# Performance work log

Hardware: AMD Instinct MI355X
Metric: run time of the kernel (lower is better)

## Reference

```python
import jax, jax.numpy as jnp
import numpy as np

EMB_DIM = 2048
NHEADS = 16
KVHEADS = 4
D_KQ = 128
D_V = 128


def setup_inputs() -> dict:
    key = jax.random.key(0)
    ks = jax.random.split(key, 7)
    B, S = 2, 2048
    std = 0.02
    return {
        "q": jax.random.normal(ks[0], (B, S, EMB_DIM), jnp.float32),
        "k": jax.random.normal(ks[1], (B, S, EMB_DIM), jnp.float32),
        "v": jax.random.normal(ks[2], (B, S, EMB_DIM), jnp.float32),
        # weights stored [in, out] (transposed vs torch nn.Linear storage)
        "Wq": jax.random.normal(ks[3], (EMB_DIM, NHEADS * D_KQ), jnp.float32) * std,
        "Wk": jax.random.normal(ks[4], (EMB_DIM, KVHEADS * D_KQ), jnp.float32) * std,
        "Wv": jax.random.normal(ks[5], (EMB_DIM, KVHEADS * D_V), jnp.float32) * std,
        "Wo": jax.random.normal(ks[6], (NHEADS * D_V, EMB_DIM), jnp.float32) * std,
    }


def reference(q, k, v, Wq, Wk, Wv, Wo):
    B, S, _ = q.shape
    scale = D_KQ ** -0.25  # applied to both q and k -> combined 1/sqrt(d_kq)
    # per-head projections: [B, H, S, d]
    qh = (q @ Wq).reshape(B, S, NHEADS, D_KQ).transpose(0, 2, 1, 3) * scale
    kh = (k @ Wk).reshape(B, S, KVHEADS, D_KQ).transpose(0, 2, 1, 3) * scale
    vh = (v @ Wv).reshape(B, S, KVHEADS, D_V).transpose(0, 2, 1, 3)
    # GQA expansion: each kv head repeated `expansion` times consecutively
    expansion = NHEADS // KVHEADS
    kh = jnp.repeat(kh, expansion, axis=1)  # [B, H, S, d_kq]
    vh = jnp.repeat(vh, expansion, axis=1)  # [B, H, S, d_v]
    # full softmax FIRST, then causal tril mask, then renormalize (source quirk)
    scores = jax.nn.softmax(jnp.einsum("bhqd,bhkd->bhqk", qh, kh), axis=-1)
    scores = jnp.tril(scores)  # zero out strictly-upper triangle on last 2 dims
    scores = scores / (jnp.sum(scores, axis=-1, keepdims=True) + 1e-9)
    qkv = jnp.einsum("bhqk,bhkd->bhqd", scores, vh)  # [B, H, S, d_v]
    z = qkv.transpose(0, 2, 1, 3).reshape(B, S, NHEADS * D_V)
    return z @ Wo
```

## Files before the change

### kernel.cpp

```cpp
#include <hip/hip_runtime.h>

#define S_LEN 2048
#define EMB 2048
#define NH 16
#define KVH 4
#define DH 128

typedef __bf16 bf16x8 __attribute__((ext_vector_type(8)));
typedef float floatx4 __attribute__((ext_vector_type(4)));
typedef unsigned short ushortx8 __attribute__((ext_vector_type(8)));
typedef unsigned short ushortx4 __attribute__((ext_vector_type(4)));

static __device__ __forceinline__ unsigned short f2bf(float f) {
  unsigned u = __float_as_uint(f);
  return (unsigned short)((u + 0x7fffu + ((u >> 16) & 1u)) >> 16);
}

static __device__ __forceinline__ void gload16(const unsigned short* g, unsigned short* l) {
  __builtin_amdgcn_global_load_lds(
      (const __attribute__((address_space(1))) unsigned int*)(const void*)g,
      (__attribute__((address_space(3))) unsigned int*)(void*)l, 16, 0, 0);
}

__global__ __launch_bounds__(256) void pre_kernel(
    const float* __restrict__ q, const float* __restrict__ k, const float* __restrict__ v,
    const float* __restrict__ Wq, const float* __restrict__ Wk,
    const float* __restrict__ Wv, const float* __restrict__ Wo,
    unsigned short* __restrict__ qo, unsigned short* __restrict__ ko,
    unsigned short* __restrict__ vo,
    unsigned short* __restrict__ Wqt, unsigned short* __restrict__ Wkt,
    unsigned short* __restrict__ Wvt, unsigned short* __restrict__ Wot,
    float scale) {
  __shared__ float t[32][33];
  int bx = blockIdx.x;
  if (bx < 12288) {
    const int sel = bx >> 12;
    const float* in = (sel == 0) ? q : (sel == 1) ? k : v;
    unsigned short* out = (sel == 0) ? qo : (sel == 1) ? ko : vo;
    size_t i = (((size_t)(bx & 4095)) * 256 + threadIdx.x) * 8;
    floatx4 a = *(const floatx4*)(in + i);
    floatx4 bvec = *(const floatx4*)(in + i + 4);
    ushortx8 o;
    #pragma unroll
    for (int c = 0; c < 4; ++c) { o[c] = f2bf(a[c]); o[4 + c] = f2bf(bvec[c]); }
    *(ushortx8*)(out + i) = o;
  } else {
    bx -= 12288;
    const float* W; unsigned short* Wt; int N, tile; float sc;
    if (bx < 4096)      { W = Wq; Wt = Wqt; N = 2048; tile = bx;        sc = scale; }
    else if (bx < 5120) { W = Wk; Wt = Wkt; N = 512;  tile = bx - 4096; sc = scale; }
    else if (bx < 6144) { W = Wv; Wt = Wvt; N = 512;  tile = bx - 5120; sc = 1.0f; }
    else                { W = Wo; Wt = Wot; N = 2048; tile = bx - 6144; sc = 1.0f; }
    const int ntiles = N >> 5;
    const int n0 = (tile % ntiles) * 32, k0 = (tile / ntiles) * 32;
    const int tx = threadIdx.x & 31, ty = threadIdx.x >> 5;
    #pragma unroll
    for (int r = 0; r < 4; ++r)
      t[ty + r * 8][tx] = W[(size_t)(k0 + ty + r * 8) * N + n0 + tx];
    __syncthreads();
    #pragma unroll
    for (int r = 0; r < 4; ++r)
      Wt[(size_t)(n0 + ty + r * 8) * 2048 + k0 + tx] = f2bf(t[tx][ty + r * 8] * sc);
  }
}

static __device__ __forceinline__ void gemm256_core(
    const unsigned short* __restrict__ Ab, const unsigned short* __restrict__ Bb,
    bool swap, unsigned short* As, unsigned short* Bs, floatx4 (&acc)[8][4]) {
  const int tid = threadIdx.x;
  const int lane = tid & 63, w = tid >> 6;
  const int lm = lane & 15, gq = lane >> 4;
  const int wm = w >> 2, wn = w & 3;
  const int lr = lane >> 3, lc = (lane & 7) ^ lr;

  auto stageH = [&](const unsigned short* gb, unsigned short* lt, int half, int kst) {
    #pragma unroll
    for (int qq = 0; qq < 2; ++qq) {
      const int rb = half * 128 + w * 16 + qq * 8;
      gload16(gb + (((size_t)(rb + lr)) << 11) + kst + (lc << 3), lt + rb * 64);
    }
  };

  stageH(Ab, As, 0, 0);            stageH(Ab, As, 1, 0);
  stageH(Bb, Bs, 0, 0);            stageH(Bb, Bs, 1, 0);
  stageH(Ab, As + 16384, 0, 64);   stageH(Ab, As + 16384, 1, 64);
  stageH(Bb, Bs + 16384, 0, 64);   stageH(Bb, Bs + 16384, 1, 64);
  asm volatile("s_waitcnt vmcnt(8)" ::: "memory");
  __builtin_amdgcn_s_barrier();

  const int r1 = (wm * 128 + lm) * 64;
  const int r2 = (wn * 64 + lm) * 64;
  const int c0 = ((0 + gq) ^ (lm & 7)) * 8;
  const int c1 = ((4 + gq) ^ (lm & 7)) * 8;

#define TILE_BODY(AsC, BsC, KST, DOSTG)                                                         \
  {                                                                                             \
    const unsigned short* l1 = swap ? (BsC) : (AsC);                                            \
    const unsigned short* l2 = swap ? (AsC) : (BsC);                                            \
    bf16x8 op1[8], o2a[4], o2b[4];                                                              \
    _Pragma("unroll") for (int i = 0; i < 8; ++i)                                               \
      op1[i] = *(const bf16x8*)&l1[r1 + i * 1024 + c0];                                         \
    _Pragma("unroll") for (int j = 0; j < 4; ++j)                                               \
      o2a[j] = *(const bf16x8*)&l2[r2 + j * 1024 + c0];                                         \
    __builtin_amdgcn_s_barrier();                                                               \
    asm volatile("s_waitcnt lgkmcnt(0)" ::: "memory");                                          \
    __builtin_amdgcn_s_setprio(1);                                                              \
    _Pragma("unroll") for (int i = 0; i < 8; ++i) {                                             \
      acc[i][0] = __builtin_amdgcn_mfma_f32_16x16x32_bf16(op1[i], o2a[0], acc[i][0], 0, 0, 0);  \
      acc[i][1] = __builtin_amdgcn_mfma_f32_16x16x32_bf16(op1[i], o2a[1], acc[i][1], 0, 0, 0);  \
    }                                                                                           \
    __builtin_amdgcn_s_setprio(0);                                                              \
    __builtin_amdgcn_s_barrier();                                                               \
    _Pragma("unroll") for (int j = 0; j < 4; ++j)                                               \
      o2b[j] = *(const bf16x8*)&l2[r2 + j * 1024 + c1];                                         \
    __builtin_amdgcn_s_barrier();                                                               \
    asm volatile("s_waitcnt lgkmcnt(0)" ::: "memory");                                          \
    __builtin_amdgcn_s_setprio(1);                                                              \
    _Pragma("unroll") for (int i = 0; i < 8; ++i) {                                             \
      acc[i][2] = __builtin_amdgcn_mfma_f32_16x16x32_bf16(op1[i], o2a[2], acc[i][2], 0, 0, 0);  \
      acc[i][3] = __builtin_amdgcn_mfma_f32_16x16x32_bf16(op1[i], o2a[3], acc[i][3], 0, 0, 0);  \
    }                                                                                           \
    __builtin_amdgcn_s_setprio(0);                                                              \
    __builtin_amdgcn_s_barrier();                                                               \
    _Pragma("unroll") for (int i = 0; i < 8; ++i)                                               \
      op1[i] = *(const bf16x8*)&l1[r1 + i * 1024 + c1];                                         \
    __builtin_amdgcn_s_barrier();                                                               \
    asm volatile("s_waitcnt lgkmcnt(0)" ::: "memory");                                          \
    __builtin_amdgcn_s_setprio(1);                                                              \
    _Pragma("unroll") for (int i = 0; i < 8; ++i) {                                             \
      acc[i][0] = __builtin_amdgcn_mfma_f32_16x16x32_bf16(op1[i], o2b[0], acc[i][0], 0, 0, 0);  \
      acc[i][1] = __builtin_amdgcn_mfma_f32_16x16x32_bf16(op1[i], o2b[1], acc[i][1], 0, 0, 0);  \
    }                                                                                           \
    __builtin_amdgcn_s_setprio(0);                                                              \
    __builtin_amdgcn_s_barrier();                                                               \
    if (DOSTG) {                                                                                \
      stageH(Ab, (AsC), 0, (KST)); stageH(Ab, (AsC), 1, (KST));                                 \
      stageH(Bb, (BsC), 0, (KST)); stageH(Bb, (BsC), 1, (KST));                                 \
    }                                                                                           \
    __builtin_amdgcn_s_barrier();                                                               \
    __builtin_amdgcn_s_setprio(1);                                                              \
    _Pragma("unroll") for (int i = 0; i < 8; ++i) {                                             \
      acc[i][2] = __builtin_amdgcn_mfma_f32_16x16x32_bf16(op1[i], o2b[2], acc[i][2], 0, 0, 0);  \
      acc[i][3] = __builtin_amdgcn_mfma_f32_16x16x32_bf16(op1[i], o2b[3], acc[i][3], 0, 0, 0);  \
    }                                                                                           \
    __builtin_amdgcn_s_setprio(0);                                                              \
    if (DOSTG) { asm volatile("s_waitcnt vmcnt(8)" ::: "memory"); }                             \
    else       { asm volatile("s_waitcnt vmcnt(0)" ::: "memory"); }                             \
    __builtin_amdgcn_s_barrier();                                                               \
  }

  #pragma unroll 1
  for (int t = 0; t < 30; t += 2) {
    TILE_BODY(As, Bs, (t + 2) * 64, 1);
    TILE_BODY(As + 16384, Bs + 16384, (t + 3) * 64, 1);
  }
  TILE_BODY(As, Bs, 0, 0);
  TILE_BODY(As + 16384, Bs + 16384, 0, 0);
#undef TILE_BODY
}

__global__ __launch_bounds__(512, 2) void proj_kernel(
    const unsigned short* __restrict__ qb, const unsigned short* __restrict__ kb,
    const unsigned short* __restrict__ vb,
    const unsigned short* __restrict__ Wqt, const unsigned short* __restrict__ Wkt,
    const unsigned short* __restrict__ Wvt,
    unsigned short* __restrict__ Qh, unsigned short* __restrict__ Kh,
    unsigned short* __restrict__ Vt) {
  extern __shared__ unsigned short lds[];
  unsigned short* As = lds;
  unsigned short* Bs = lds + 32768;
  int bid = (int)blockIdx.x;
  bid = (bid & 7) * 24 + (bid >> 3);
  const unsigned short *Ab, *Bb;
  int task, bn, bt;
  if (bid < 128)      { task = 0; bn = bid >> 4;         bt = bid & 15;         Ab = qb; Bb = Wqt; }
  else if (bid < 160) { task = 1; bn = (bid - 128) >> 4; bt = (bid - 128) & 15; Ab = kb; Bb = Wkt; }
  else                { task = 2; bn = (bid - 160) >> 4; bt = (bid - 160) & 15; Ab = vb; Bb = Wvt; }
  Ab += ((size_t)bt) << 19;
  Bb += ((size_t)bn) << 19;

  floatx4 acc[8][4] = {};
  gemm256_core(Ab, Bb, task != 2, As, Bs, acc);

  const int tid = threadIdx.x, lane = tid & 63, w = tid >> 6;
  const int lm = lane & 15, gq = lane >> 4;
  const int wm = w >> 2, wn = w & 3;
  if (task != 2) {
    unsigned short* outp = (task == 0) ? Qh : Kh;
    const int nheads = (task == 0) ? NH : KVH;
    const int head = bn * 2 + wm;
    #pragma unroll
    for (int i = 0; i < 8; ++i) {
      const int d0 = i * 16 + gq * 4;
      #pragma unroll
      for (int j = 0; j < 4; ++j) {
        const int tg = bt * 256 + wn * 64 + j * 16 + lm;
        const int b_ = tg >> 11, s_ = tg & 2047;
        ushortx4 pk;
        #pragma unroll
        for (int r = 0; r < 4; ++r) pk[r] = f2bf(acc[i][j][r]);
        *(ushortx4*)&outp[((size_t)(b_ * nheads + head) * S_LEN + s_) * DH + d0] = pk;
      }
    }
  } else {
    #pragma unroll
    for (int i = 0; i < 8; ++i) {
      const int sgl = bt * 256 + wm * 128 + i * 16 + gq * 4;
      const int b_ = sgl >> 11, s_ = sgl & 2047;
      #pragma unroll
      for (int j = 0; j < 4; ++j) {
        const int dl = wn * 64 + j * 16;
        const int head = bn * 2 + (dl >> 7);
        const int dd = (dl & 127) + lm;
        ushortx4 pk;
        #pragma unroll
        for (int r = 0; r < 4; ++r) pk[r] = f2bf(acc[i][j][r]);
        *(ushortx4*)&Vt[((size_t)(b_ * KVH + head) * DH + dd) * S_LEN + s_] = pk;
      }
    }
  }
}

__global__ __launch_bounds__(512, 2) void out_kernel(const unsigned short* __restrict__ Z,
                                                     const unsigned short* __restrict__ Wot,
                                                     float* __restrict__ outp) {
  extern __shared__ unsigned short lds[];
  unsigned short* As = lds;
  unsigned short* Bs = lds + 32768;
  int bid = (int)blockIdx.x;
  bid = (bid & 7) * 16 + (bid >> 3);
  const int bn = bid >> 4, bt = bid & 15;

  floatx4 acc[8][4] = {};
  gemm256_core(Z + (((size_t)bt) << 19), Wot + (((size_t)bn) << 19), true, As, Bs, acc);

  const int tid = threadIdx.x, lane = tid & 63, w = tid >> 6;
  const int lm = lane & 15, gq = lane >> 4;
  const int wm = w >> 2, wn = w & 3;
  #pragma unroll
  for (int i = 0; i < 8; ++i) {
    const int n0 = bn * 256 + wm * 128 + i * 16 + gq * 4;
    #pragma unroll
    for (int j = 0; j < 4; ++j) {
      const int tg = bt * 256 + wn * 64 + j * 16 + lm;
      *(floatx4*)&outp[(size_t)tg * 2048 + n0] = acc[i][j];
    }
  }
}

__global__ __launch_bounds__(256) void attn_kernel(const unsigned short* __restrict__ Qh,
                                                   const unsigned short* __restrict__ Kh,
                                                   const unsigned short* __restrict__ Vt,
                                                   unsigned short* __restrict__ Z) {
  __shared__ unsigned short Ks[64][136];
  __shared__ unsigned short Vs[128][72];
  __shared__ unsigned short Ps[4][16][80];
  const int tid = threadIdx.x;
  const int w = tid >> 6, lane = tid & 63;
  const int lm = lane & 15, gq = lane >> 4;
  const int h = blockIdx.y, b = blockIdx.z;
  const unsigned short* Kp = Kh + (size_t)(b * KVH + (h >> 2)) * S_LEN * DH;
  const unsigned short* Vp = Vt + (size_t)(b * KVH + (h >> 2)) * DH * S_LEN;

  const int krow = tid >> 2, kq4 = tid & 3;
  const int vd = tid >> 1, vhf = tid & 1;

  ushortx8 kreg[4], vreg[4];
  {
    const unsigned short* ks = Kp + (size_t)krow * DH + kq4 * 32;
    const unsigned short* vs = Vp + (size_t)vd * S_LEN + vhf * 32;
    #pragma unroll
    for (int i = 0; i < 4; ++i) { kreg[i] = *(const ushortx8*)(ks + i * 8); vreg[i] = *(const ushortx8*)(vs + i * 8); }
  }

  bf16x8 ones;
  #pragma unroll
  for (int c = 0; c < 8; ++c) ones[c] = (__bf16)1.0f;

  #pragma unroll 1
  for (int pass = 0; pass < 2; ++pass) {
    const int qt = pass ? (int)blockIdx.x : 31 - (int)blockIdx.x;
    const int Q0 = qt * 64;
    const unsigned short* Qp = Qh + ((size_t)(b * NH + h) * S_LEN + Q0) * DH;
    bf16x8 qfr[4];
    #pragma unroll
    for (int kk = 0; kk < 4; ++kk)
      qfr[kk] = *(const bf16x8*)(Qp + (size_t)(w * 16 + lm) * DH + kk * 32 + gq * 8);

    floatx4 acc_o[8] = {};
    floatx4 acc_l = {};

    for (int it = 0; it <= qt; ++it) {
      const int kv0 = it * 64;
      __syncthreads();
      #pragma unroll
      for (int i = 0; i < 4; ++i) *(ushortx8*)&Ks[krow][kq4 * 32 + i * 8] = kreg[i];
      #pragma unroll
      for (int i = 0; i < 4; ++i) *(ushortx8*)&Vs[vd][vhf * 32 + i * 8] = vreg[i];
      __syncthreads();
      if (!(pass == 1 && it == qt)) {
        const int kvn = (it < qt) ? kv0 + 64 : 0;
        const unsigned short* ks = Kp + (size_t)(kvn + krow) * DH + kq4 * 32;
        const unsigned short* vs = Vp + (size_t)vd * S_LEN + kvn + vhf * 32;
        #pragma unroll
        for (int i = 0; i < 4; ++i) { kreg[i] = *(const ushortx8*)(ks + i * 8); vreg[i] = *(const ushortx8*)(vs + i * 8); }
      }
      floatx4 sa[4] = {};
      #pragma unroll
      for (int j = 0; j < 4; ++j)
        #pragma unroll
        for (int kk = 0; kk < 4; ++kk) {
          bf16x8 bk = *(const bf16x8*)&Ks[j * 16 + lm][kk * 32 + gq * 8];
          sa[j] = __builtin_amdgcn_mfma_f32_16x16x32_bf16(qfr[kk], bk, sa[j], 0, 0, 0);
        }
      const int rowb = Q0 + w * 16 + gq * 4;
      #pragma unroll
      for (int r = 0; r < 4; ++r) {
        const int qg = rowb + r;
        #pragma unroll
        for (int j = 0; j < 4; ++j) {
          const int kg = kv0 + j * 16 + lm;
          const float p = (kg <= qg) ? __expf(sa[j][r]) : 0.0f;
          Ps[w][gq * 4 + r][j * 16 + lm] = f2bf(p);
        }
      }
      bf16x8 ap0 = *(const bf16x8*)&Ps[w][lm][gq * 8];
      bf16x8 ap1 = *(const bf16x8*)&Ps[w][lm][32 + gq * 8];
      #pragma unroll
      for (int jd = 0; jd < 8; ++jd) {
        bf16x8 bv0 = *(const bf16x8*)&Vs[jd * 16 + lm][gq * 8];
        bf16x8 bv1 = *(const bf16x8*)&Vs[jd * 16 + lm][32 + gq * 8];
        acc_o[jd] = __builtin_amdgcn_mfma_f32_16x16x32_bf16(bv0, ap0, acc_o[jd], 0, 0, 0);
        acc_o[jd] = __builtin_amdgcn_mfma_f32_16x16x32_bf16(bv1, ap1, acc_o[jd], 0, 0, 0);
      }
      acc_l = __builtin_amdgcn_mfma_f32_16x16x32_bf16(ones, ap0, acc_l, 0, 0, 0);
      acc_l = __builtin_amdgcn_mfma_f32_16x16x32_bf16(ones, ap1, acc_l, 0, 0, 0);
    }

    const float inv = 1.0f / acc_l[0];
    const size_t t_ = (size_t)b * S_LEN + Q0 + w * 16 + lm;
    #pragma unroll
    for (int jd = 0; jd < 8; ++jd) {
      ushortx4 pk;
      #pragma unroll
      for (int r = 0; r < 4; ++r) pk[r] = f2bf(acc_o[jd][r] * inv);
      *(ushortx4*)&Z[t_ * (NH * DH) + h * DH + jd * 16 + gq * 4] = pk;
    }
  }
}

extern "C" void kernel_launch(void* const* d_in, const int* in_sizes, int n_in,
                              void* d_out, int out_size, void* d_ws, size_t ws_size,
                              hipStream_t stream) {
  (void)in_sizes; (void)n_in; (void)out_size; (void)ws_size;
  const float* q  = (const float*)d_in[0];
  const float* k  = (const float*)d_in[1];
  const float* v  = (const float*)d_in[2];
  const float* Wq = (const float*)d_in[3];
  const float* Wk = (const float*)d_in[4];
  const float* Wv = (const float*)d_in[5];
  const float* Wo = (const float*)d_in[6];

  unsigned short* Qh  = (unsigned short*)d_ws;
  unsigned short* Kh  = Qh + (size_t)2 * NH * S_LEN * DH;
  unsigned short* Vt  = Kh + (size_t)2 * KVH * S_LEN * DH;
  unsigned short* Z   = Vt + (size_t)2 * KVH * S_LEN * DH;
  unsigned short* vb  = Z + (size_t)4096 * 2048;
  unsigned short* Wqt = vb + (size_t)4096 * 2048;
  unsigned short* Wkt = Wqt + (size_t)2048 * 2048;
  unsigned short* Wvt = Wkt + (size_t)512 * 2048;
  unsigned short* Wot = Wvt + (size_t)512 * 2048;
  unsigned short* qb = (unsigned short*)d_out;
  unsigned short* kb = qb + (size_t)4096 * 2048;

  const float scale = 0.29730177875068026f;

  static int s_attr_done = 0;
  if (!s_attr_done) {
    hipFuncSetAttribute(reinterpret_cast<const void*>(proj_kernel),
                        hipFuncAttributeMaxDynamicSharedMemorySize, 131072);
    hipFuncSetAttribute(reinterpret_cast<const void*>(out_kernel),
                        hipFuncAttributeMaxDynamicSharedMemorySize, 131072);
    s_attr_done = 1;
  }

  pre_kernel<<<22528, 256, 0, stream>>>(q, k, v, Wq, Wk, Wv, Wo,
                                        qb, kb, vb, Wqt, Wkt, Wvt, Wot, scale);
  proj_kernel<<<192, 512, 131072, stream>>>(qb, kb, vb, Wqt, Wkt, Wvt, Qh, Kh, Vt);
  attn_kernel<<<dim3(16, 16, 2), 256, 0, stream>>>(Qh, Kh, Vt, Z);
  out_kernel<<<128, 512, 131072, stream>>>(Z, Wot, (float*)d_out);
}
```

Baseline: 373.2 us.

## Spread GEMM tile staging across MFMA phases and pad attention P buffer

The GEMM main loop no longer issues all four global-to-LDS loads for the next K-tile in one burst. It now spreads the loads across the four MFMA sub-phases, staggered between the two LDS buffers, with tighter vmcnt waits, so memory traffic overlaps compute more evenly. The attention kernel pads its P scratch row stride from 80 to 88 to reduce LDS bank conflicts, and uses the native bf16 conversion instead of manual rounding. The new staging order depends on careful buffer-reuse timing, so a hazard between the stores into one buffer and the reads still being made from it could cause races.

Measured after the change: 355.8 us. 1.05x faster.

```diff
diff --git a/kernel.cpp b/kernel.cpp
--- a/kernel.cpp
+++ b/kernel.cpp
@@ -81,11 +81,13 @@
     }
   };
 
-  stageH(Ab, As, 0, 0);            stageH(Ab, As, 1, 0);
-  stageH(Bb, Bs, 0, 0);            stageH(Bb, Bs, 1, 0);
-  stageH(Ab, As + 16384, 0, 64);   stageH(Ab, As + 16384, 1, 64);
-  stageH(Bb, Bs + 16384, 0, 64);   stageH(Bb, Bs + 16384, 1, 64);
-  asm volatile("s_waitcnt vmcnt(8)" ::: "memory");
+  unsigned short* As2 = As + 16384;
+  unsigned short* Bs2 = Bs + 16384;
+
+  stageH(Ab, As, 0, 0);  stageH(Ab, As, 1, 0);
+  stageH(Bb, Bs, 0, 0);  stageH(Bb, Bs, 1, 0);
+  stageH(Ab, As2, 0, 64);
+  asm volatile("s_waitcnt vmcnt(2)" ::: "memory");
   __builtin_amdgcn_s_barrier();
 
   const int r1 = (wm * 128 + lm) * 64;
@@ -93,15 +95,16 @@
   const int c0 = ((0 + gq) ^ (lm & 7)) * 8;
   const int c1 = ((4 + gq) ^ (lm & 7)) * 8;
 
-#define TILE_BODY(AsC, BsC, KST, DOSTG)                                                         \
+#define TILE_BODY(CA, CB, OA, OB, KS1, KS2, STG1, STG4)                                         \
   {                                                                                             \
-    const unsigned short* l1 = swap ? (BsC) : (AsC);                                            \
-    const unsigned short* l2 = swap ? (AsC) : (BsC);                                            \
+    const unsigned short* l1 = swap ? (CB) : (CA);                                              \
+    const unsigned short* l2 = swap ? (CA) : (CB);                                              \
     bf16x8 op1[8], o2a[4], o2b[4];                                                              \
     _Pragma("unroll") for (int i = 0; i < 8; ++i)                                               \
       op1[i] = *(const bf16x8*)&l1[r1 + i * 1024 + c0];                                         \
     _Pragma("unroll") for (int j = 0; j < 4; ++j)                                               \
       o2a[j] = *(const bf16x8*)&l2[r2 + j * 1024 + c0];                                         \
+    if (STG1) stageH(Ab, (OA), 1, (KS1));                                                       \
     __builtin_amdgcn_s_barrier();                                                               \
     asm volatile("s_waitcnt lgkmcnt(0)" ::: "memory");                                          \
     __builtin_amdgcn_s_setprio(1);                                                              \
@@ -113,6 +116,7 @@
     __builtin_amdgcn_s_barrier();                                                               \
     _Pragma("unroll") for (int j = 0; j < 4; ++j)                                               \
       o2b[j] = *(const bf16x8*)&l2[r2 + j * 1024 + c1];                                         \
+    if (STG1) stageH(Bb, (OB), 0, (KS1));                                                       \
     __builtin_amdgcn_s_barrier();                                                               \
     asm volatile("s_waitcnt lgkmcnt(0)" ::: "memory");                                          \
     __builtin_amdgcn_s_setprio(1);                                                              \
@@ -124,6 +128,7 @@
     __builtin_amdgcn_s_barrier();                                                               \
     _Pragma("unroll") for (int i = 0; i < 8; ++i)                                               \
       op1[i] = *(const bf16x8*)&l1[r1 + i * 1024 + c1];                                         \
+    if (STG1) stageH(Bb, (OB), 1, (KS1));                                                       \
     __builtin_amdgcn_s_barrier();                                                               \
     asm volatile("s_waitcnt lgkmcnt(0)" ::: "memory");                                          \
     __builtin_amdgcn_s_setprio(1);                                                              \
@@ -133,10 +138,7 @@
     }                                                                                           \
     __builtin_amdgcn_s_setprio(0);                                                              \
     __builtin_amdgcn_s_barrier();                                                               \
-    if (DOSTG) {                                                                                \
-      stageH(Ab, (AsC), 0, (KST)); stageH(Ab, (AsC), 1, (KST));                                 \
-      stageH(Bb, (BsC), 0, (KST)); stageH(Bb, (BsC), 1, (KST));                                 \
-    }                                                                                           \
+    if (STG4) stageH(Ab, (CA), 0, (KS2));                                                       \
     __builtin_amdgcn_s_barrier();                                                               \
     __builtin_amdgcn_s_setprio(1);                                                              \
     _Pragma("unroll") for (int i = 0; i < 8; ++i) {                                             \
@@ -144,18 +146,18 @@
       acc[i][3] = __builtin_amdgcn_mfma_f32_16x16x32_bf16(op1[i], o2b[3], acc[i][3], 0, 0, 0);  \
     }                                                                                           \
     __builtin_amdgcn_s_setprio(0);                                                              \
-    if (DOSTG) { asm volatile("s_waitcnt vmcnt(8)" ::: "memory"); }                             \
-    else       { asm volatile("s_waitcnt vmcnt(0)" ::: "memory"); }                             \
+    if (STG4) { asm volatile("s_waitcnt vmcnt(2)" ::: "memory"); }                              \
+    else      { asm volatile("s_waitcnt vmcnt(0)" ::: "memory"); }                              \
     __builtin_amdgcn_s_barrier();                                                               \
   }
 
   #pragma unroll 1
   for (int t = 0; t < 30; t += 2) {
-    TILE_BODY(As, Bs, (t + 2) * 64, 1);
-    TILE_BODY(As + 16384, Bs + 16384, (t + 3) * 64, 1);
-  }
-  TILE_BODY(As, Bs, 0, 0);
-  TILE_BODY(As + 16384, Bs + 16384, 0, 0);
+    TILE_BODY(As, Bs, As2, Bs2, (t + 1) * 64, (t + 2) * 64, 1, 1);
+    TILE_BODY(As2, Bs2, As, Bs, (t + 2) * 64, (t + 3) * 64, 1, 1);
+  }
+  TILE_BODY(As, Bs, As2, Bs2, 31 * 64, 0, 1, 0);
+  TILE_BODY(As2, Bs2, As, Bs, 0, 0, 0, 0);
 #undef TILE_BODY
 }
 
@@ -254,7 +256,7 @@
                                                    unsigned short* __restrict__ Z) {
   __shared__ unsigned short Ks[64][136];
   __shared__ unsigned short Vs[128][72];
-  __shared__ unsigned short Ps[4][16][80];
+  __shared__ unsigned short Ps[4][16][88];
   const int tid = threadIdx.x;
   const int w = tid >> 6, lane = tid & 63;
   const int lm = lane & 15, gq = lane >> 4;
@@ -321,7 +323,7 @@
         for (int j = 0; j < 4; ++j) {
           const int kg = kv0 + j * 16 + lm;
           const float p = (kg <= qg) ? __expf(sa[j][r]) : 0.0f;
-          Ps[w][gq * 4 + r][j * 16 + lm] = f2bf(p);
+          Ps[w][gq * 4 + r][j * 16 + lm] = __builtin_bit_cast(unsigned short, (__bf16)p);
         }
       }
       bf16x8 ap0 = *(const bf16x8*)&Ps[w][lm][gq * 8];
```
